# Performance work log

Measured on AMD Instinct MI355X. Metric: run time of the kernel, lower is better.

The kernel has to match this reference:

```python
import jax, jax.numpy as jnp
import numpy as np

T, B, IN_DIM, H, N_RESETS = 4096, 256, 128, 8, 32


def setup_inputs() -> dict:
    key = jax.random.key(0)
    ks = jax.random.split(key, 8)
    s = 1.0 / np.sqrt(H)  # PyTorch LSTM/Linear init scale
    return {
        "x": jax.random.normal(ks[0], (T, B, IN_DIM), jnp.float32),
        "reset_idx": jnp.sort(jax.random.randint(ks[1], (N_RESETS,), 0, T)),
        "W_ih": jax.random.uniform(ks[2], (4 * H, IN_DIM), jnp.float32, -s, s),
        "W_hh": jax.random.uniform(ks[3], (4 * H, H), jnp.float32, -s, s),
        "b_ih": jax.random.uniform(ks[4], (4 * H,), jnp.float32, -s, s),
        "b_hh": jax.random.uniform(ks[5], (4 * H,), jnp.float32, -s, s),
        "W_proj": jax.random.uniform(ks[6], (1, H), jnp.float32, -s, s),
        "b_proj": jax.random.uniform(ks[7], (1,), jnp.float32, -s, s),
    }


def reference(x, reset_idx, W_ih, W_hh, b_ih, b_hh, W_proj, b_proj):
    # x: [T, B, in_dim] (batch_first=False).  reset_idx: timesteps where the
    # LSTM hidden/cell state is reset to zero before processing that step.
    Tn = x.shape[0]
    Bn = x.shape[1]
    Hn = W_hh.shape[1]
    reset_mask = jnp.zeros((Tn,), dtype=bool).at[reset_idx].set(True)

    # Precompute the input contribution to the gates for all timesteps at once
    # (this is the bulk of the FLOPs; only the small HxH recurrence stays in scan).
    x_gates = jnp.einsum("tbi,gi->tbg", x, W_ih) + b_ih + b_hh  # [T, B, 4H]

    def step(carry, inp):
        h, c = carry  # [B, H] each
        xg, rt = inp  # [B, 4H], scalar bool
        h = jnp.where(rt, jnp.zeros_like(h), h)
        c = jnp.where(rt, jnp.zeros_like(c), c)
        gates = xg + h @ W_hh.T  # [B, 4H]
        i, f, g, o = jnp.split(gates, 4, axis=-1)  # PyTorch gate order i,f,g,o
        c = jax.nn.sigmoid(f) * c + jax.nn.sigmoid(i) * jnp.tanh(g)
        h = jax.nn.sigmoid(o) * jnp.tanh(c)
        return (h, c), h

    h0 = jnp.zeros((Bn, Hn), x.dtype)
    c0 = jnp.zeros((Bn, Hn), x.dtype)
    (_, _), rnn_out = jax.lax.scan(step, (h0, c0), (x_gates, reset_mask))

    value = rnn_out @ W_proj.T + b_proj  # [T, B, 1]
    return (value, rnn_out)
```

## Files before the change

### kernel.cpp

```cpp
#include <hip/hip_runtime.h>
#include <cstdint>

#define TT 4096
#define BB 256
#define ID 128

typedef float f32x4 __attribute__((ext_vector_type(4)));
typedef short s16x8 __attribute__((ext_vector_type(8)));

__device__ __forceinline__ float rcp_fast(float x) { return __builtin_amdgcn_rcpf(x); }
__device__ __forceinline__ float sigm(float x) { return rcp_fast(1.0f + __expf(-x)); }
__device__ __forceinline__ float tanh_fast(float x) {
  float e = __expf(2.0f * x);
  return 1.0f - 2.0f * rcp_fast(e + 1.0f);
}

union U16B { uint32_t u[4]; s16x8 v; };

__device__ __forceinline__ void split8(const float4 a, const float4 b,
                                       s16x8& hi, s16x8& lo) {
  uint32_t a0 = __float_as_uint(a.x), a1 = __float_as_uint(a.y);
  uint32_t a2 = __float_as_uint(a.z), a3 = __float_as_uint(a.w);
  uint32_t b0 = __float_as_uint(b.x), b1 = __float_as_uint(b.y);
  uint32_t b2 = __float_as_uint(b.z), b3 = __float_as_uint(b.w);
  U16B h;
  h.u[0] = (a0 >> 16) | (a1 & 0xffff0000u);
  h.u[1] = (a2 >> 16) | (a3 & 0xffff0000u);
  h.u[2] = (b0 >> 16) | (b1 & 0xffff0000u);
  h.u[3] = (b2 >> 16) | (b3 & 0xffff0000u);
  hi = h.v;
  float r0 = a.x - __uint_as_float(a0 & 0xffff0000u);
  float r1 = a.y - __uint_as_float(a1 & 0xffff0000u);
  float r2 = a.z - __uint_as_float(a2 & 0xffff0000u);
  float r3 = a.w - __uint_as_float(a3 & 0xffff0000u);
  float r4 = b.x - __uint_as_float(b0 & 0xffff0000u);
  float r5 = b.y - __uint_as_float(b1 & 0xffff0000u);
  float r6 = b.z - __uint_as_float(b2 & 0xffff0000u);
  float r7 = b.w - __uint_as_float(b3 & 0xffff0000u);
  U16B l;
  l.u[0] = (__float_as_uint(r0) >> 16) | (__float_as_uint(r1) & 0xffff0000u);
  l.u[1] = (__float_as_uint(r2) >> 16) | (__float_as_uint(r3) & 0xffff0000u);
  l.u[2] = (__float_as_uint(r4) >> 16) | (__float_as_uint(r5) & 0xffff0000u);
  l.u[3] = (__float_as_uint(r6) >> 16) | (__float_as_uint(r7) & 0xffff0000u);
  lo = l.v;
}

__global__ __launch_bounds__(256) void gates_kernel(
    const float* __restrict__ x, const float* __restrict__ W_ih,
    const float* __restrict__ b_ih, const float* __restrict__ b_hh,
    float* __restrict__ xg)
{
  __shared__ float4 xt[64 * 32];
  __shared__ float4 wt[32 * 32];
  const int tid = threadIdx.x;
  const size_t row0 = (size_t)blockIdx.x * 64;

  const float4* __restrict__ src = reinterpret_cast<const float4*>(x) + row0 * 32;
#pragma unroll
  for (int it = 0; it < 8; ++it) {
    int idx = it * 256 + tid;
    int r = idx >> 5, q = idx & 31;
    xt[r * 32 + (q ^ (r & 31))] = src[idx];
  }
  const float4* __restrict__ wsrc = reinterpret_cast<const float4*>(W_ih);
#pragma unroll
  for (int it = 0; it < 4; ++it) {
    int idx = it * 256 + tid;
    int g = idx >> 5, q = idx & 31;
    wt[g * 32 + (q ^ (g & 31))] = wsrc[idx];
  }
  __syncthreads();

  const int lane = tid & 63;
  const int wv   = tid >> 6;
  const int rloc = wv * 16 + (lane & 15);
  const int kq   = (lane >> 4) * 2;

  s16x8 Bh[4][2], Bl[4][2];
#pragma unroll
  for (int kc = 0; kc < 4; ++kc) {
#pragma unroll
    for (int nf = 0; nf < 2; ++nf) {
      int g = nf * 16 + (lane & 15);
      int q0 = kc * 8 + kq;
      float4 wa = wt[g * 32 + (q0 ^ (g & 31))];
      float4 wb = wt[g * 32 + ((q0 + 1) ^ (g & 31))];
      split8(wa, wb, Bh[kc][nf], Bl[kc][nf]);
    }
  }

  f32x4 acc[2] = {{0.f, 0.f, 0.f, 0.f}, {0.f, 0.f, 0.f, 0.f}};
#pragma unroll
  for (int kc = 0; kc < 4; ++kc) {
    int q0 = kc * 8 + kq;
    float4 xa = xt[rloc * 32 + (q0 ^ (rloc & 31))];
    float4 xb = xt[rloc * 32 + ((q0 + 1) ^ (rloc & 31))];
    s16x8 Ah, Al;
    split8(xa, xb, Ah, Al);
#pragma unroll
    for (int nf = 0; nf < 2; ++nf) {
      acc[nf] = __builtin_amdgcn_mfma_f32_16x16x32_bf16(Ah, Bh[kc][nf], acc[nf], 0, 0, 0);
      acc[nf] = __builtin_amdgcn_mfma_f32_16x16x32_bf16(Ah, Bl[kc][nf], acc[nf], 0, 0, 0);
      acc[nf] = __builtin_amdgcn_mfma_f32_16x16x32_bf16(Al, Bh[kc][nf], acc[nf], 0, 0, 0);
    }
  }

#pragma unroll
  for (int nf = 0; nf < 2; ++nf) {
    int g = nf * 16 + (lane & 15);
    float bo = b_ih[g] + b_hh[g];
    size_t rowg = row0 + wv * 16 + (lane >> 4) * 4;
#pragma unroll
    for (int reg = 0; reg < 4; ++reg) {
      xg[(rowg + reg) * 32 + g] = acc[nf][reg] + bo;
    }
  }
}

__global__ __launch_bounds__(64) void rnn_kernel(
    const float* __restrict__ xg, const int* __restrict__ reset_idx,
    const float* __restrict__ W_hh, const float* __restrict__ W_proj,
    const float* __restrict__ b_proj, float* __restrict__ out)
{
  const int seg  = blockIdx.x;
  const int lane = threadIdx.x;
  const int j    = lane & 7;
  const int b    = blockIdx.y * 8 + (lane >> 3);

  const int start = (seg == 0)  ? 0  : reset_idx[seg - 1];
  const int end   = (seg == 32) ? TT : reset_idx[seg];
  if (start >= end) return;

  float wi[8], wf[8], wg_[8], wo[8];
#pragma unroll
  for (int k = 0; k < 8; ++k) {
    wi[k]  = W_hh[(0  + j) * 8 + k];
    wf[k]  = W_hh[(8  + j) * 8 + k];
    wg_[k] = W_hh[(16 + j) * 8 + k];
    wo[k]  = W_hh[(24 + j) * 8 + k];
  }
  const float bp = b_proj[0];
  float wp[8];
#pragma unroll
  for (int k = 0; k < 8; ++k) wp[k] = W_proj[k];

  float h[8];
#pragma unroll
  for (int k = 0; k < 8; ++k) h[k] = 0.f;
  float c = 0.f;

  float* __restrict__ vout = out;
  float* __restrict__ hout = out + (size_t)TT * BB;

  float bufA[32], bufB[32];

#define LOADC(buf, tc) do {                                                  \
  _Pragma("unroll")                                                          \
  for (int s = 0; s < 8; ++s) {                                              \
    int tt = (tc) + s; tt = tt < TT ? tt : TT - 1;   \
    size_t ba = ((size_t)tt * BB + b) * 32 + j;                              \
    (buf)[s*4+0] = xg[ba];      (buf)[s*4+1] = xg[ba + 8];                   \
    (buf)[s*4+2] = xg[ba + 16]; (buf)[s*4+3] = xg[ba + 24];                  \
  }                                                                          \
} while (0)

#define STEP8(buf, tc) do {                                                  \
  _Pragma("unroll")                                                          \
  for (int s = 0; s < 8; ++s) {                                              \
    int t = (tc) + s;                                                        \
    if (t < end) {                                  \
      float gi = (buf)[s*4+0], gf = (buf)[s*4+1];                            \
      float gg = (buf)[s*4+2], go = (buf)[s*4+3];                            \
      float gi1 = 0.f, gf1 = 0.f, gg1 = 0.f, go1 = 0.f;                      \
      _Pragma("unroll")                                                      \
      for (int k = 0; k < 8; k += 2) {                                       \
        gi += wi[k]  * h[k];  gi1 += wi[k+1]  * h[k+1];                      \
        gf += wf[k]  * h[k];  gf1 += wf[k+1]  * h[k+1];                      \
        gg += wg_[k] * h[k];  gg1 += wg_[k+1] * h[k+1];                      \
        go += wo[k]  * h[k];  go1 += wo[k+1]  * h[k+1];                      \
      }                                                                      \
      gi += gi1; gf += gf1; gg += gg1; go += go1;                            \
      float si = sigm(gi), sf = sigm(gf), sg = tanh_fast(gg), so = sigm(go); \
      c = sf * c + si * sg;                                                  \
      float hj = so * tanh_fast(c);                                          \
      hout[((size_t)t * BB + b) * 8 + j] = hj;                               \
      _Pragma("unroll")                                                      \
      for (int k = 0; k < 8; ++k) h[k] = __shfl(hj, k, 8);                   \
      float sv = bp;                                                         \
      _Pragma("unroll")                                                      \
      for (int k = 0; k < 8; ++k) sv += wp[k] * h[k];                        \
      if (j == 0) vout[(size_t)t * BB + b] = sv;                             \
    }                                                                        \
  }                                                                          \
} while (0)

  LOADC(bufA, start);
  LOADC(bufB, start + 8);
  for (int tc = start; tc < end; tc += 16) {
    STEP8(bufA, tc);
    LOADC(bufA, tc + 16);
    STEP8(bufB, tc + 8);
    LOADC(bufB, tc + 24);
  }
#undef LOADC
#undef STEP8
}

extern "C" void kernel_launch(void* const* d_in, const int* in_sizes, int n_in,
                              void* d_out, int out_size, void* d_ws, size_t ws_size,
                              hipStream_t stream) {
  const float* x      = (const float*)d_in[0];
  const int*   ridx   = (const int*)  d_in[1];
  const float* W_ih   = (const float*)d_in[2];
  const float* W_hh   = (const float*)d_in[3];
  const float* b_ih   = (const float*)d_in[4];
  const float* b_hh   = (const float*)d_in[5];
  const float* W_proj = (const float*)d_in[6];
  const float* b_proj = (const float*)d_in[7];
  float* out = (float*)d_out;
  float* xg  = (float*)d_ws;

  gates_kernel<<<(TT * BB) / 64, 256, 0, stream>>>(x, W_ih, b_ih, b_hh, xg);
  rnn_kernel<<<dim3(33, 32), 64, 0, stream>>>(xg, ridx, W_hh, W_proj, b_proj, out);
}
```

Baseline: 252.9 us.

## Interleave gate layout for float4 loads in recurrence; drop LDS staging in GEMM

The gates kernel now reads x and W_ih directly from global memory instead of staging them through swizzled shared memory, and it writes the gate outputs in an interleaved layout with the four gates of each hidden unit adjacent. The recurrent kernel can then fetch all four gate values for a timestep with one float4 load instead of four scalar loads. The aim is fewer load instructions on the latency-bound sequential scan, plus removal of the LDS round trip and barrier in the GEMM. The cost is uncoalesced strided global reads in the GEMM and scattered output stores.

New measurement: 317.2 us. 25.4% more time.

```diff
diff --git a/kernel.cpp b/kernel.cpp
--- a/kernel.cpp
+++ b/kernel.cpp
@@ -50,51 +50,36 @@
     const float* __restrict__ b_ih, const float* __restrict__ b_hh,
     float* __restrict__ xg)
 {
-  __shared__ float4 xt[64 * 32];
-  __shared__ float4 wt[32 * 32];
-  const int tid = threadIdx.x;
-  const size_t row0 = (size_t)blockIdx.x * 64;
-
-  const float4* __restrict__ src = reinterpret_cast<const float4*>(x) + row0 * 32;
-#pragma unroll
-  for (int it = 0; it < 8; ++it) {
-    int idx = it * 256 + tid;
-    int r = idx >> 5, q = idx & 31;
-    xt[r * 32 + (q ^ (r & 31))] = src[idx];
-  }
-  const float4* __restrict__ wsrc = reinterpret_cast<const float4*>(W_ih);
-#pragma unroll
-  for (int it = 0; it < 4; ++it) {
-    int idx = it * 256 + tid;
-    int g = idx >> 5, q = idx & 31;
-    wt[g * 32 + (q ^ (g & 31))] = wsrc[idx];
-  }
-  __syncthreads();
-
+  const int tid  = threadIdx.x;
   const int lane = tid & 63;
   const int wv   = tid >> 6;
+  const size_t row0 = (size_t)blockIdx.x * 64;
   const int rloc = wv * 16 + (lane & 15);
   const int kq   = (lane >> 4) * 2;
 
+  const float4* __restrict__ x4 = reinterpret_cast<const float4*>(x);
+  const float4* __restrict__ w4 = reinterpret_cast<const float4*>(W_ih);
+
   s16x8 Bh[4][2], Bl[4][2];
 #pragma unroll
   for (int kc = 0; kc < 4; ++kc) {
 #pragma unroll
     for (int nf = 0; nf < 2; ++nf) {
-      int g = nf * 16 + (lane & 15);
+      int g  = nf * 16 + (lane & 15);
       int q0 = kc * 8 + kq;
-      float4 wa = wt[g * 32 + (q0 ^ (g & 31))];
-      float4 wb = wt[g * 32 + ((q0 + 1) ^ (g & 31))];
+      float4 wa = w4[g * 32 + q0];
+      float4 wb = w4[g * 32 + q0 + 1];
       split8(wa, wb, Bh[kc][nf], Bl[kc][nf]);
     }
   }
 
   f32x4 acc[2] = {{0.f, 0.f, 0.f, 0.f}, {0.f, 0.f, 0.f, 0.f}};
+  const size_t xbase = (row0 + (size_t)rloc) * 32;
 #pragma unroll
   for (int kc = 0; kc < 4; ++kc) {
     int q0 = kc * 8 + kq;
-    float4 xa = xt[rloc * 32 + (q0 ^ (rloc & 31))];
-    float4 xb = xt[rloc * 32 + ((q0 + 1) ^ (rloc & 31))];
+    float4 xa = x4[xbase + q0];
+    float4 xb = x4[xbase + q0 + 1];
     s16x8 Ah, Al;
     split8(xa, xb, Ah, Al);
 #pragma unroll
@@ -109,10 +94,11 @@
   for (int nf = 0; nf < 2; ++nf) {
     int g = nf * 16 + (lane & 15);
     float bo = b_ih[g] + b_hh[g];
+    int off = (g & 7) * 4 + (g >> 3);
     size_t rowg = row0 + wv * 16 + (lane >> 4) * 4;
 #pragma unroll
     for (int reg = 0; reg < 4; ++reg) {
-      xg[(rowg + reg) * 32 + g] = acc[nf][reg] + bo;
+      xg[(rowg + reg) * 32 + off] = acc[nf][reg] + bo;
     }
   }
 }
@@ -152,15 +138,16 @@
   float* __restrict__ vout = out;
   float* __restrict__ hout = out + (size_t)TT * BB;
 
-  float bufA[32], bufB[32];
+  const float4* __restrict__ xg4 = reinterpret_cast<const float4*>(xg);
+  const size_t lbase = (size_t)b * 8 + j;
+
+  float4 bufA[8], bufB[8];
 
 #define LOADC(buf, tc) do {                                                  \
   _Pragma("unroll")                                                          \
   for (int s = 0; s < 8; ++s) {                                              \
     int tt = (tc) + s; tt = tt < TT ? tt : TT - 1;   \
-    size_t ba = ((size_t)tt * BB + b) * 32 + j;                              \
-    (buf)[s*4+0] = xg[ba];      (buf)[s*4+1] = xg[ba + 8];                   \
-    (buf)[s*4+2] = xg[ba + 16]; (buf)[s*4+3] = xg[ba + 24];                  \
+    (buf)[s] = xg4[(size_t)tt * 2048 + lbase];                               \
   }                                                                          \
 } while (0)
 
@@ -169,8 +156,8 @@
   for (int s = 0; s < 8; ++s) {                                              \
     int t = (tc) + s;                                                        \
     if (t < end) {                                  \
-      float gi = (buf)[s*4+0], gf = (buf)[s*4+1];                            \
-      float gg = (buf)[s*4+2], go = (buf)[s*4+3];                            \
+      float gi = (buf)[s].x, gf = (buf)[s].y;                                \
+      float gg = (buf)[s].z, go = (buf)[s].w;                                \
       float gi1 = 0.f, gf1 = 0.f, gg1 = 0.f, go1 = 0.f;                      \
       _Pragma("unroll")                                                      \
       for (int k = 0; k < 8; k += 2) {                                       \
```
